# Performance work log

Measured on AMD Instinct MI355X. Metric: run time of the kernel, lower is better.

The kernel has to match this reference:

```python
import jax, jax.numpy as jnp
import numpy as np

B, N, T, D, H, E = 2, 1024, 8, 128, 4, 8192
DH = D // H
NEG_SLOPE = 0.2  # GATv2Conv default negative_slope


def _ln(x, g, b):
    m = jnp.mean(x, -1, keepdims=True)
    v = jnp.mean((x - m) ** 2, -1, keepdims=True)
    return (x - m) * jax.lax.rsqrt(v + 1e-5) * g + b


def _forward(x, edge_index, gat_wl, gat_wr, gat_att, gat_b, in_w, in_b, out_w, out_b,
             ffn_w1, ffn_b1, ffn_w2, ffn_b2, fus_w, fus_b,
             lns_g, lns_b, lnt1_g, lnt1_b, lnt2_g, lnt2_b, lnf_g, lnf_b):
    # ---- spatial branch: GATv2, vectorized over (B, T) instead of python loops ----
    loops = jnp.arange(N)
    src = jnp.concatenate([edge_index[0], loops])  # j: message source (PyG adds self loops)
    dst = jnp.concatenate([edge_index[1], loops])  # i: aggregation target
    xl = jnp.einsum('bntd,de->bnte', x, gat_wl).reshape(B, N, T, H, D)
    xr = jnp.einsum('bntd,de->bnte', x, gat_wr).reshape(B, N, T, H, D)
    ml = xl[:, src]                                  # [B,Et,T,H,D]
    mr = xr[:, dst]
    e = jax.nn.leaky_relu(ml + mr, NEG_SLOPE)
    logits = jnp.einsum('bethd,hd->beth', e, gat_att)
    logits = jnp.moveaxis(logits, 1, 0)              # [Et,B,T,H]
    mx = jax.ops.segment_max(logits, dst, num_segments=N)
    p = jnp.exp(logits - mx[dst])                    # stable edge softmax per dst node
    ssum = jax.ops.segment_sum(p, dst, num_segments=N)
    alpha = p / ssum[dst]                            # [Et,B,T,H]
    msg = alpha[..., None] * jnp.moveaxis(ml, 1, 0)
    agg = jax.ops.segment_sum(msg, dst, num_segments=N)  # [N,B,T,H,D]
    x_sp = jnp.moveaxis(agg.mean(3), 0, 1) + gat_b   # concat=False -> head mean; [B,N,T,D]
    x_sp = _ln(x_sp, lns_g, lns_b)

    # ---- temporal branch: MHA + FFN, vectorized over all B*N nodes ----
    xt = x.reshape(B * N, T, D)
    qkv = xt @ in_w + in_b
    q, k, v = jnp.split(qkv, 3, axis=-1)
    q = q.reshape(B * N, T, H, DH)
    k = k.reshape(B * N, T, H, DH)
    v = v.reshape(B * N, T, H, DH)
    scores = jnp.einsum('bthd,bshd->bhts', q, k) / np.float32(np.sqrt(DH))
    attn = jax.nn.softmax(scores, -1)
    o = jnp.einsum('bhts,bshd->bthd', attn, v).reshape(B * N, T, D)
    o = o @ out_w + out_b
    x1 = _ln(xt + o, lnt1_g, lnt1_b)
    ffn = jax.nn.gelu(x1 @ ffn_w1 + ffn_b1, approximate=False) @ ffn_w2 + ffn_b2
    x_tp = _ln(x1 + ffn, lnt2_g, lnt2_b).reshape(B, N, T, D)

    # ---- gated fusion with residual ----
    g = jax.nn.sigmoid(jnp.concatenate([x_sp, x_tp], -1) @ fus_w + fus_b)
    return _ln(g * x_sp + (1.0 - g) * x_tp + x, lnf_g, lnf_b)


def setup_inputs() -> dict:
    key = jax.random.key(0)
    ks = jax.random.split(key, 12)
    s = 0.05
    f = jnp.float32
    return {
        'x': jax.random.normal(ks[0], (B, N, T, D), f),
        'edge_index': jax.random.randint(ks[1], (2, E), 0, N),
        'gat_wl': jax.random.normal(ks[2], (D, H * D), f) * s,
        'gat_wr': jax.random.normal(ks[3], (D, H * D), f) * s,
        'gat_att': jax.random.normal(ks[4], (H, D), f) * s,
        'gat_b': jnp.zeros((D,), f),
        'in_w': jax.random.normal(ks[5], (D, 3 * D), f) * s,
        'in_b': jnp.zeros((3 * D,), f),
        'out_w': jax.random.normal(ks[6], (D, D), f) * s,
        'out_b': jnp.zeros((D,), f),
        'ffn_w1': jax.random.normal(ks[7], (D, 4 * D), f) * s,
        'ffn_b1': jnp.zeros((4 * D,), f),
        'ffn_w2': jax.random.normal(ks[8], (4 * D, D), f) * s,
        'ffn_b2': jnp.zeros((D,), f),
        'fus_w': jax.random.normal(ks[9], (2 * D, D), f) * s,
        'fus_b': jnp.zeros((D,), f),
        'lns_g': jnp.ones((D,), f), 'lns_b': jnp.zeros((D,), f),
        'lnt1_g': jnp.ones((D,), f), 'lnt1_b': jnp.zeros((D,), f),
        'lnt2_g': jnp.ones((D,), f), 'lnt2_b': jnp.zeros((D,), f),
        'lnf_g': jnp.ones((D,), f), 'lnf_b': jnp.zeros((D,), f),
    }


def reference(x, edge_index, gat_wl, gat_wr, gat_att, gat_b, in_w, in_b, out_w, out_b,
              ffn_w1, ffn_b1, ffn_w2, ffn_b2, fus_w, fus_b,
              lns_g, lns_b, lnt1_g, lnt1_b, lnt2_g, lnt2_b, lnf_g, lnf_b):
    return _forward(x, edge_index, gat_wl, gat_wr, gat_att, gat_b, in_w, in_b, out_w, out_b,
                    ffn_w1, ffn_b1, ffn_w2, ffn_b2, fus_w, fus_b,
                    lns_g, lns_b, lnt1_g, lnt1_b, lnt2_g, lnt2_b, lnf_g, lnf_b)
```

## Files before the change

### kernel.cpp

```cpp
#include <hip/hip_runtime.h>
#include <math.h>

#define B_ 2
#define N_ 1024
#define T_ 8
#define D_ 128
#define H_ 4
#define E_ 8192
#define EN_ 9216
#define M_ 16384

typedef unsigned short u16;
using bf16x8 = __attribute__((ext_vector_type(8))) short;
using f32x4  = __attribute__((ext_vector_type(4))) float;

__device__ __forceinline__ float bf2f(unsigned int u) {
  return __uint_as_float(u << 16);
}
__device__ __forceinline__ u16 f2bf(float f) {
  unsigned int x = __float_as_uint(f);
  x += 0x7fffu + ((x >> 16) & 1u);
  return (u16)(x >> 16);
}
__device__ __forceinline__ void load8f(const u16* p, float* f) {
  uint4 u = *(const uint4*)p;
  f[0]=bf2f(u.x & 0xffffu); f[1]=bf2f(u.x >> 16);
  f[2]=bf2f(u.y & 0xffffu); f[3]=bf2f(u.y >> 16);
  f[4]=bf2f(u.z & 0xffffu); f[5]=bf2f(u.z >> 16);
  f[6]=bf2f(u.w & 0xffffu); f[7]=bf2f(u.w >> 16);
}
__device__ __forceinline__ void unpack8(uint4 u, float* f) {
  f[0]=bf2f(u.x & 0xffffu); f[1]=bf2f(u.x >> 16);
  f[2]=bf2f(u.y & 0xffffu); f[3]=bf2f(u.y >> 16);
  f[4]=bf2f(u.z & 0xffffu); f[5]=bf2f(u.z >> 16);
  f[6]=bf2f(u.w & 0xffffu); f[7]=bf2f(u.w >> 16);
}
__device__ __forceinline__ void gl2lds(const u16* g, u16* l) {
  __builtin_amdgcn_global_load_lds(
      (const __attribute__((address_space(1))) unsigned int*)(const void*)g,
      (__attribute__((address_space(3))) unsigned int*)(void*)l,
      16, 0, 0);
}

__device__ __forceinline__ u16 conv_w_elem(int idx,
    const float* wl, const float* wr, const float* inw, const float* outw,
    const float* f1, const float* f2, const float* fw) {
  const float* src; int base, K, N;
  if      (idx < 65536)  { src = wl;   base = 0;      K = 128; N = 512; }
  else if (idx < 131072) { src = wr;   base = 65536;  K = 128; N = 512; }
  else if (idx < 180224) { src = inw;  base = 131072; K = 128; N = 384; }
  else if (idx < 196608) { src = outw; base = 180224; K = 128; N = 128; }
  else if (idx < 262144) { src = f1;   base = 196608; K = 128; N = 512; }
  else if (idx < 327680) { src = f2;   base = 262144; K = 512; N = 128; }
  else                   { src = fw;   base = 327680; K = 256; N = 128; }
  int o = idx - base;
  int n = o / K, k = o - n * K;
  return f2bf(src[k * N + n]);
}

__global__ __launch_bounds__(1024) void prep_csr_k(const float* __restrict__ x,
    const float* __restrict__ wl, const float* __restrict__ wr,
    const float* __restrict__ inw, const float* __restrict__ outw,
    const float* __restrict__ f1, const float* __restrict__ f2,
    const float* __restrict__ fw,
    u16* __restrict__ XB, u16* __restrict__ WB,
    const int* __restrict__ ei, int* __restrict__ offs, int* __restrict__ srcs) {
  __shared__ int cnt[N_];
  __shared__ int cur[N_];
  int bi = blockIdx.x;
  int tid = threadIdx.x;
  if (bi < 512) {
    int i = (bi * 1024 + tid) * 4;
    float4 v = *(const float4*)&x[i];
    u16 o[4] = {f2bf(v.x), f2bf(v.y), f2bf(v.z), f2bf(v.w)};
    *(ushort4*)&XB[i] = *(ushort4*)o;
    return;
  }
  if (bi < 600) {
    int base = (bi - 512) * 4096 + tid * 4;
#pragma unroll
    for (int j = 0; j < 4; ++j)
      WB[base + j] = conv_w_elem(base + j, wl, wr, inw, outw, f1, f2, fw);
    return;
  }
  cnt[tid] = 0;
  __syncthreads();
  for (int e = tid; e < EN_; e += 1024) {
    int d = (e < E_) ? ei[E_ + e] : (e - E_);
    atomicAdd(&cnt[d], 1);
  }
  __syncthreads();
  int mine = cnt[tid];
  for (int off = 1; off < 1024; off <<= 1) {
    int tv = (tid >= off) ? cnt[tid - off] : 0;
    __syncthreads();
    cnt[tid] += tv;
    __syncthreads();
  }
  int excl = cnt[tid] - mine;
  offs[tid] = excl;
  if (tid == 1023) offs[N_] = cnt[1023];
  cur[tid] = excl;
  __syncthreads();
  for (int e = tid; e < EN_; e += 1024) {
    int d = (e < E_) ? ei[E_ + e] : (e - E_);
    int s = (e < E_) ? ei[e] : (e - E_);
    int pos = atomicAdd(&cur[d], 1);
    srcs[pos] = s;
  }
}

template<int BM, int ACT, int ROUTE>
__device__ __forceinline__ void gemm_tile(int bx, int by,
    const u16* A, int lda, const u16* WT, int K, const float* bias,
    u16* C, int ldc, u16* R0, u16* R1, u16* R2, const float* b2,
    u16* As, u16* Bs) {
  constexpr int MI = BM / 32;
  int tid = threadIdx.x;
  int lane = tid & 63, wid = tid >> 6;
  int lr = lane & 15, lk = lane >> 4;
  int wm = (wid >> 1) * (BM / 2);
  int wn = (wid & 1) * 64;

  u16* Cb; int ldc_; int col0; const float* bias_;
  if (ROUTE) {
    if (bx < 4)      { Cb = R0; ldc_ = 512; col0 = bx * 128;       bias_ = nullptr; }
    else if (bx < 8) { Cb = R1; ldc_ = 512; col0 = (bx - 4) * 128; bias_ = nullptr; }
    else             { Cb = R2; ldc_ = 384; col0 = (bx - 8) * 128; bias_ = b2; }
  } else { Cb = C; ldc_ = ldc; col0 = bx * 128; bias_ = bias; }

  f32x4 acc[MI][4] = {};
  for (int k0 = 0; k0 < K; k0 += 32) {
    __syncthreads();
#pragma unroll
    for (int i = 0; i < BM / 64; ++i) {
      int o = tid * 16 + i * 4096;
      int row = o >> 6;
      int col = (o >> 1) & 31;
      gl2lds(A + (size_t)(by * BM + row) * lda + k0 + col,
             (u16*)((char*)As + wid * 1024 + i * 4096));
    }
#pragma unroll
    for (int i = 0; i < 2; ++i) {
      int o = tid * 16 + i * 4096;
      int nrow = o >> 6;
      int col = (o >> 1) & 31;
      gl2lds(WT + (size_t)(bx * 128 + nrow) * K + k0 + col,
             (u16*)((char*)Bs + wid * 1024 + i * 4096));
    }
    __syncthreads();
    bf16x8 bf[4];
#pragma unroll
    for (int ni = 0; ni < 4; ++ni)
      bf[ni] = *(const bf16x8*)&Bs[(wn + ni * 16 + lr) * 32 + lk * 8];
#pragma unroll
    for (int mi = 0; mi < MI; ++mi) {
      bf16x8 af = *(const bf16x8*)&As[(wm + mi * 16 + lr) * 32 + lk * 8];
#pragma unroll
      for (int ni = 0; ni < 4; ++ni)
        acc[mi][ni] = __builtin_amdgcn_mfma_f32_16x16x32_bf16(af, bf[ni], acc[mi][ni], 0, 0, 0);
    }
  }
  float bc[4];
#pragma unroll
  for (int ni = 0; ni < 4; ++ni)
    bc[ni] = bias_ ? bias_[col0 + wn + ni * 16 + lr] : 0.f;
#pragma unroll
  for (int mi = 0; mi < MI; ++mi) {
#pragma unroll
    for (int r = 0; r < 4; ++r) {
      int row = by * BM + wm + mi * 16 + lk * 4 + r;
#pragma unroll
      for (int ni = 0; ni < 4; ++ni) {
        int col = col0 + wn + ni * 16 + lr;
        float v = acc[mi][ni][r] + bc[ni];
        if (ACT) v = 0.5f * v * (1.f + erff(v * 0.70710678118f));
        Cb[(size_t)row * ldc_ + col] = f2bf(v);
      }
    }
  }
}

template<int EPI>
__device__ __forceinline__ void ln_epilogue(int by, f32x4 (&acc)[2][4],
    const float* bias, const float* xres, const u16* xcat,
    const float* lng, const float* lnb,
    float* o32, u16* o16, int os16, float* rs, float* rq) {
  int tid = threadIdx.x;
  int lane = tid & 63, wid = tid >> 6;
  int lr = lane & 15, lk = lane >> 4;
  int wm = (wid >> 1) * 32, wn = (wid & 1) * 64;
  float bc[4];
#pragma unroll
  for (int ni = 0; ni < 4; ++ni) bc[ni] = bias[wn + ni * 16 + lr];
#pragma unroll
  for (int mi = 0; mi < 2; ++mi) {
#pragma unroll
    for (int r = 0; r < 4; ++r) {
      int row = by * 64 + wm + mi * 16 + lk * 4 + r;
      float s = 0.f, s2 = 0.f;
#pragma unroll
      for (int ni = 0; ni < 4; ++ni) {
        int col = wn + ni * 16 + lr;
        float v = acc[mi][ni][r] + bc[ni];
        if (EPI == 1 || EPI == 2) {
          v += xres[(size_t)row * 128 + col];
        } else {
          float gg = 1.f / (1.f + __expf(-v));
          float xsp = bf2f(xcat[(size_t)row * 256 + col]);
          float xtp = bf2f(xcat[(size_t)row * 256 + 128 + col]);
          v = gg * xsp + (1.f - gg) * xtp + xres[(size_t)row * 128 + col];
        }
        acc[mi][ni][r] = v;
        s += v; s2 += v * v;
      }
      s += __shfl_xor(s, 1, 64); s2 += __shfl_xor(s2, 1, 64);
      s += __shfl_xor(s, 2, 64); s2 += __shfl_xor(s2, 2, 64);
      s += __shfl_xor(s, 4, 64); s2 += __shfl_xor(s2, 4, 64);
      s += __shfl_xor(s, 8, 64); s2 += __shfl_xor(s2, 8, 64);
      if (lr == 0) {
        int rl = wm + mi * 16 + lk * 4 + r;
        rs[rl * 2 + (wid & 1)] = s;
        rq[rl * 2 + (wid & 1)] = s2;
      }
    }
  }
  __syncthreads();
#pragma unroll
  for (int mi = 0; mi < 2; ++mi) {
#pragma unroll
    for (int r = 0; r < 4; ++r) {
      int rl = wm + mi * 16 + lk * 4 + r;
      int row = by * 64 + rl;
      float tot = rs[rl * 2] + rs[rl * 2 + 1];
      float tq = rq[rl * 2] + rq[rl * 2 + 1];
      float mean = tot * (1.f / 128.f);
      float var = tq * (1.f / 128.f) - mean * mean;
      float rinv = rsqrtf(var + 1e-5f);
#pragma unroll
      for (int ni = 0; ni < 4; ++ni) {
        int col = wn + ni * 16 + lr;
        float o = (acc[mi][ni][r] - mean) * rinv * lng[col] + lnb[col];
        if (EPI != 2) o32[(size_t)row * 128 + col] = o;
        if (EPI != 3) o16[(size_t)row * os16 + col] = f2bf(o);
      }
    }
  }
}

__global__ __launch_bounds__(256) void fusion_k(const u16* __restrict__ A,
    const u16* __restrict__ WT, const float* __restrict__ bias,
    const float* __restrict__ xres, const u16* __restrict__ xcat,
    const float* __restrict__ lng, const float* __restrict__ lnb,
    float* __restrict__ o32) {
  __shared__ u16 As[64 * 32];
  __shared__ u16 Bs[128 * 32];
  __shared__ float rs[128], rq[128];
  int by = blockIdx.x;
  int tid = threadIdx.x;
  int lane = tid & 63, wid = tid >> 6;
  int lr = lane & 15, lk = lane >> 4;
  int wm = (wid >> 1) * 32, wn = (wid & 1) * 64;
  const int K = 256;

  f32x4 acc[2][4] = {};
  for (int k0 = 0; k0 < K; k0 += 32) {
    __syncthreads();
    {
      int o = tid * 16;
      gl2lds(A + (size_t)(by * 64 + (o >> 6)) * K + k0 + ((o >> 1) & 31),
             (u16*)((char*)As + wid * 1024));
    }
#pragma unroll
    for (int i = 0; i < 2; ++i) {
      int o = tid * 16 + i * 4096;
      gl2lds(WT + (size_t)(o >> 6) * K + k0 + ((o >> 1) & 31),
             (u16*)((char*)Bs + wid * 1024 + i * 4096));
    }
    __syncthreads();
    bf16x8 bf[4];
#pragma unroll
    for (int ni = 0; ni < 4; ++ni)
      bf[ni] = *(const bf16x8*)&Bs[(wn + ni * 16 + lr) * 32 + lk * 8];
#pragma unroll
    for (int mi = 0; mi < 2; ++mi) {
      bf16x8 af = *(const bf16x8*)&As[(wm + mi * 16 + lr) * 32 + lk * 8];
#pragma unroll
      for (int ni = 0; ni < 4; ++ni)
        acc[mi][ni] = __builtin_amdgcn_mfma_f32_16x16x32_bf16(af, bf[ni], acc[mi][ni], 0, 0, 0);
    }
  }
  ln_epilogue<3>(by, acc, bias, xres, xcat, lng, lnb, o32, nullptr, 0, rs, rq);
}

__global__ __launch_bounds__(256) void proj_k(const u16* __restrict__ XB,
    const u16* __restrict__ WT1, const float* __restrict__ in_b,
    u16* __restrict__ XL, u16* __restrict__ XR, u16* __restrict__ QKV) {
  __shared__ u16 As[128 * 32];
  __shared__ u16 Bs[128 * 32];
  gemm_tile<128, 0, 1>(blockIdx.x, blockIdx.y, XB, 128, WT1, 128, nullptr,
                       nullptr, 0, XL, XR, QKV, in_b, As, Bs);
}

__global__ __launch_bounds__(256) void gat_k(const u16* __restrict__ XL,
    const u16* __restrict__ XR,
    const int* __restrict__ offs, const int* __restrict__ srcs,
    const float* __restrict__ att, const float* __restrict__ gb,
    const float* __restrict__ lng, const float* __restrict__ lnb,
    u16* __restrict__ XCAT) {
  int w = blockIdx.x * 4 + (threadIdx.x >> 6);
  int lane = threadIdx.x & 63;
  int n = w >> 4;
  int b = (w >> 3) & 1;
  int t = w & 7;
  int dd = (lane & 15) * 8;
  size_t tokn = (size_t)(b * N_ + n) * 8 + t;
  size_t rowoff = (size_t)b * (N_ * 8) + t;

  float mr[8], av[8];
  load8f(XR + tokn * 512 + lane * 8, mr);
  *(float4*)&av[0] = *(const float4*)(att + lane * 8);
  *(float4*)&av[4] = *(const float4*)(att + lane * 8 + 4);

  int beg = offs[n], end = offs[n + 1];
  float sH = 0.f;
  float acc[8] = {0.f, 0.f, 0.f, 0.f, 0.f, 0.f, 0.f, 0.f};
  int i = beg;
  uint4 r0 = *(const uint4*)(XL + (rowoff + (size_t)srcs[i] * 8) * 512 + lane * 8);
  uint4 r1 = r0;
  if (i + 1 < end)
    r1 = *(const uint4*)(XL + (rowoff + (size_t)srcs[i + 1] * 8) * 512 + lane * 8);
  while (i + 1 < end) {
    uint4 c0 = r0, c1 = r1;
    if (i + 2 < end)
      r0 = *(const uint4*)(XL + (rowoff + (size_t)srcs[i + 2] * 8) * 512 + lane * 8);
    if (i + 3 < end)
      r1 = *(const uint4*)(XL + (rowoff + (size_t)srcs[i + 3] * 8) * 512 + lane * 8);
    float ml0[8], ml1[8];
    unpack8(c0, ml0);
    unpack8(c1, ml1);
    float d0 = 0.f, d1 = 0.f;
#pragma unroll
    for (int j = 0; j < 8; ++j) {
      float m0 = ml0[j] + mr[j];
      m0 = fmaxf(m0, 0.2f * m0);
      d0 += m0 * av[j];
      float m1 = ml1[j] + mr[j];
      m1 = fmaxf(m1, 0.2f * m1);
      d1 += m1 * av[j];
    }
    d0 += __shfl_xor(d0, 1, 64); d1 += __shfl_xor(d1, 1, 64);
    d0 += __shfl_xor(d0, 2, 64); d1 += __shfl_xor(d1, 2, 64);
    d0 += __shfl_xor(d0, 4, 64); d1 += __shfl_xor(d1, 4, 64);
    d0 += __shfl_xor(d0, 8, 64); d1 += __shfl_xor(d1, 8, 64);
    float p0 = __expf(d0), p1 = __expf(d1);
    sH += p0 + p1;
#pragma unroll
    for (int j = 0; j < 8; ++j) acc[j] += p0 * ml0[j] + p1 * ml1[j];
    i += 2;
  }
  if (i < end) {
    float ml0[8];
    unpack8(r0, ml0);
    float d0 = 0.f;
#pragma unroll
    for (int j = 0; j < 8; ++j) {
      float m0 = ml0[j] + mr[j];
      m0 = fmaxf(m0, 0.2f * m0);
      d0 += m0 * av[j];
    }
    d0 += __shfl_xor(d0, 1, 64);
    d0 += __shfl_xor(d0, 2, 64);
    d0 += __shfl_xor(d0, 4, 64);
    d0 += __shfl_xor(d0, 8, 64);
    float p0 = __expf(d0);
    sH += p0;
#pragma unroll
    for (int j = 0; j < 8; ++j) acc[j] += p0 * ml0[j];
  }
  float invS = 1.f / sH;
#pragma unroll
  for (int j = 0; j < 8; ++j) acc[j] *= invS;
#pragma unroll
  for (int j = 0; j < 8; ++j) {
    acc[j] += __shfl_xor(acc[j], 16, 64);
    acc[j] += __shfl_xor(acc[j], 32, 64);
  }
#pragma unroll
  for (int j = 0; j < 8; ++j) acc[j] = acc[j] * 0.25f + gb[dd + j];
  float s = 0.f, s2 = 0.f;
#pragma unroll
  for (int j = 0; j < 8; ++j) { s += acc[j]; s2 += acc[j] * acc[j]; }
#pragma unroll
  for (int m = 1; m < 16; m <<= 1) {
    s += __shfl_xor(s, m, 64);
    s2 += __shfl_xor(s2, m, 64);
  }
  float mean = s * (1.f / 128.f);
  float var = s2 * (1.f / 128.f) - mean * mean;
  float r = rsqrtf(var + 1e-5f);
  if (lane < 16) {
    u16 ob[8];
#pragma unroll
    for (int j = 0; j < 8; ++j)
      ob[j] = f2bf((acc[j] - mean) * r * lng[dd + j] + lnb[dd + j]);
    *(uint4*)&XCAT[tokn * 256 + dd] = *(uint4*)ob;
  }
}

__global__ __launch_bounds__(256) void attn_oproj_k(const u16* __restrict__ QKV,
    const u16* __restrict__ WTO, const float* __restrict__ out_b,
    const float* __restrict__ x,
    const float* __restrict__ lnt1_g, const float* __restrict__ lnt1_b,
    float* __restrict__ X1, u16* __restrict__ X1B) {
  __shared__ u16 As[4 * 64 * 32];
  __shared__ u16 Bs[4 * 128 * 32];
  __shared__ float rs[128], rq[128];
  int by = blockIdx.x;
  int tid = threadIdx.x;
  int lane = tid & 63, wid = tid >> 6;

#pragma unroll
  for (int i = 0; i < 8; ++i) {
    int o = tid * 16 + i * 4096;
    int c = o >> 13;
    int wb = o & 8191;
    int nrow = wb >> 6;
    int kin = (wb & 63) >> 1;
    gl2lds(WTO + (size_t)nrow * 128 + c * 32 + kin,
           (u16*)((char*)Bs + wid * 1024 + i * 4096));
  }

  int t = lane >> 3, sidx = lane & 7, dg = lane & 7;
  for (int it = 0; it < 8; ++it) {
    int task = wid * 8 + it;
    int bnl = task >> 2, h = task & 3;
    int bn = by * 8 + bnl;
    const u16* base = QKV + (size_t)bn * 8 * 384;
    float va[8][4];
#pragma unroll
    for (int s2 = 0; s2 < 8; ++s2) {
      ushort4 vv = *(const ushort4*)(base + s2 * 384 + 256 + h * 32 + dg * 4);
      va[s2][0] = bf2f(vv.x); va[s2][1] = bf2f(vv.y);
      va[s2][2] = bf2f(vv.z); va[s2][3] = bf2f(vv.w);
    }
    const u16* qp = base + t * 384 + h * 32;
    const u16* kp = base + sidx * 384 + 128 + h * 32;
    float sc = 0.f;
#pragma unroll
    for (int d0 = 0; d0 < 32; d0 += 8) {
      float q[8], k[8];
      load8f(qp + d0, q);
      load8f(kp + d0, k);
#pragma unroll
      for (int j = 0; j < 8; ++j) sc += q[j] * k[j];
    }
    sc *= 0.17677669529663687f;
    float m = sc;
    m = fmaxf(m, __shfl_xor(m, 1, 64));
    m = fmaxf(m, __shfl_xor(m, 2, 64));
    m = fmaxf(m, __shfl_xor(m, 4, 64));
    float p = __expf(sc - m);
    float S = p;
    S += __shfl_xor(S, 1, 64);
    S += __shfl_xor(S, 2, 64);
    S += __shfl_xor(S, 4, 64);
    float alpha = p / S;
    int tb = lane & 56;
    float o0 = 0.f, o1 = 0.f, o2 = 0.f, o3 = 0.f;
#pragma unroll
    for (int s2 = 0; s2 < 8; ++s2) {
      float a = __shfl(alpha, tb + s2, 64);
      o0 += a * va[s2][0];
      o1 += a * va[s2][1];
      o2 += a * va[s2][2];
      o3 += a * va[s2][3];
    }
    u16 ov[4] = {f2bf(o0), f2bf(o1), f2bf(o2), f2bf(o3)};
    int row = bnl * 8 + t;
    *(ushort4*)&As[h * 2048 + row * 32 + dg * 4] = *(ushort4*)ov;
  }
  __syncthreads();

  int lr = lane & 15, lk = lane >> 4;
  int wm = (wid >> 1) * 32, wn = (wid & 1) * 64;
  f32x4 acc[2][4] = {};
#pragma unroll
  for (int c = 0; c < 4; ++c) {
    bf16x8 bf[4];
#pragma unroll
    for (int ni = 0; ni < 4; ++ni)
      bf[ni] = *(const bf16x8*)&Bs[c * 4096 + (wn + ni * 16 + lr) * 32 + lk * 8];
#pragma unroll
    for (int mi = 0; mi < 2; ++mi) {
      bf16x8 af = *(const bf16x8*)&As[c * 2048 + (wm + mi * 16 + lr) * 32 + lk * 8];
#pragma unroll
      for (int ni = 0; ni < 4; ++ni)
        acc[mi][ni] = __builtin_amdgcn_mfma_f32_16x16x32_bf16(af, bf[ni], acc[mi][ni], 0, 0, 0);
    }
  }
  ln_epilogue<1>(by, acc, out_b, x, nullptr, lnt1_g, lnt1_b, X1, X1B, 128, rs, rq);
}

__global__ __launch_bounds__(256) void ffn_fused_k(const u16* __restrict__ X1B,
    const u16* __restrict__ WTF1, const u16* __restrict__ WTF2,
    const float* __restrict__ b1, const float* __restrict__ b2,
    const float* __restrict__ X1,
    const float* __restrict__ lng, const float* __restrict__ lnb,
    u16* __restrict__ XCATr) {
  __shared__ u16 As[64 * 128];
  __shared__ u16 B1s[64 * 128];
  __shared__ u16 B2s[128 * 64];
  __shared__ u16 Hc[2 * 64 * 40];
  __shared__ float rs[128], rq[128];
  int by = blockIdx.x;
  int tid = threadIdx.x;
  int lane = tid & 63, wid = tid >> 6;
  int lr = lane & 15, lk = lane >> 4;

#pragma unroll
  for (int kc = 0; kc < 4; ++kc) {
    gl2lds(X1B + (size_t)(by * 64 + (tid >> 2)) * 128 + kc * 32 + (tid & 3) * 8,
           (u16*)((char*)As + kc * 4096 + wid * 1024));
  }
  int wr0 = (wid >> 1) * 32, wc0 = (wid & 1) * 32;
  int wm = (wid >> 1) * 32, wn = (wid & 1) * 64;
  f32x4 acc2[2][4] = {};
  for (int nc = 0; nc < 8; ++nc) {
    __syncthreads();
#pragma unroll
    for (int kc = 0; kc < 4; ++kc) {
      gl2lds(WTF1 + (size_t)(nc * 64 + (tid >> 2)) * 128 + kc * 32 + (tid & 3) * 8,
             (u16*)((char*)B1s + kc * 4096 + wid * 1024));
    }
#pragma unroll
    for (int i = 0; i < 4; ++i) {
      int o = tid * 16 + i * 4096;
      int kc2l = o >> 13;
      int wb = o & 8191;
      int nrow = wb >> 6;
      int kin = (wb & 63) >> 1;
      gl2lds(WTF2 + (size_t)nrow * 512 + nc * 64 + kc2l * 32 + kin,
             (u16*)((char*)B2s + wid * 1024 + i * 4096));
    }
    __syncthreads();
    f32x4 a1[2][2] = {};
#pragma unroll
    for (int kc = 0; kc < 4; ++kc) {
      bf16x8 bf0 = *(const bf16x8*)&B1s[kc * 2048 + (wc0 + lr) * 32 + lk * 8];
      bf16x8 bf1 = *(const bf16x8*)&B1s[kc * 2048 + (wc0 + 16 + lr) * 32 + lk * 8];
#pragma unroll
      for (int mi = 0; mi < 2; ++mi) {
        bf16x8 af = *(const bf16x8*)&As[kc * 2048 + (wr0 + mi * 16 + lr) * 32 + lk * 8];
        a1[mi][0] = __builtin_amdgcn_mfma_f32_16x16x32_bf16(af, bf0, a1[mi][0], 0, 0, 0);
        a1[mi][1] = __builtin_amdgcn_mfma_f32_16x16x32_bf16(af, bf1, a1[mi][1], 0, 0, 0);
      }
    }
#pragma unroll
    for (int mi = 0; mi < 2; ++mi) {
#pragma unroll
      for (int r = 0; r < 4; ++r) {
        int row = wr0 + mi * 16 + lk * 4 + r;
#pragma unroll
        for (int ni = 0; ni < 2; ++ni) {
          int cl = wc0 + ni * 16 + lr;
          float v = a1[mi][ni][r] + b1[nc * 64 + cl];
          v = 0.5f * v * (1.f + erff(v * 0.70710678118f));
          Hc[(cl >> 5) * 2560 + row * 40 + (cl & 31)] = f2bf(v);
        }
      }
    }
    __syncthreads();
#pragma unroll
    for (int kc2l = 0; kc2l < 2; ++kc2l) {
      bf16x8 bf[4];
#pragma unroll
      for (int ni = 0; ni < 4; ++ni)
        bf[ni] = *(const bf16x8*)&B2s[kc2l * 4096 + (wn + ni * 16 + lr) * 32 + lk * 8];
#pragma unroll
      for (int mi = 0; mi < 2; ++mi) {
        bf16x8 af = *(const bf16x8*)&Hc[kc2l * 2560 + (wm + mi * 16 + lr) * 40 + lk * 8];
#pragma unroll
        for (int ni = 0; ni < 4; ++ni)
          acc2[mi][ni] = __builtin_amdgcn_mfma_f32_16x16x32_bf16(af, bf[ni], acc2[mi][ni], 0, 0, 0);
      }
    }
  }
  __syncthreads();
  ln_epilogue<2>(by, acc2, b2, X1, nullptr, lng, lnb, nullptr, XCATr, 256, rs, rq);
}

extern "C" void kernel_launch(void* const* d_in, const int* in_sizes, int n_in,
                              void* d_out, int out_size, void* d_ws, size_t ws_size,
                              hipStream_t stream) {
  const float* x       = (const float*)d_in[0];
  const int*   ei      = (const int*)d_in[1];
  const float* gat_att = (const float*)d_in[4];
  const float* gat_b   = (const float*)d_in[5];
  const float* in_b    = (const float*)d_in[7];
  const float* out_b   = (const float*)d_in[9];
  const float* ffn_b1  = (const float*)d_in[11];
  const float* ffn_b2  = (const float*)d_in[13];
  const float* fus_b   = (const float*)d_in[15];
  const float* lns_g   = (const float*)d_in[16];
  const float* lns_b   = (const float*)d_in[17];
  const float* lnt1_g  = (const float*)d_in[18];
  const float* lnt1_b  = (const float*)d_in[19];
  const float* lnt2_g  = (const float*)d_in[20];
  const float* lnt2_b  = (const float*)d_in[21];
  const float* lnf_g   = (const float*)d_in[22];
  const float* lnf_b   = (const float*)d_in[23];

  char* ws = (char*)d_ws;
  u16*   WB    = (u16*)ws;
  u16*   WTO   = WB + 180224;
  u16*   WTF1  = WB + 196608;
  u16*   WTF2  = WB + 262144;
  u16*   WTFUS = WB + 327680;
  int*   OFFS  = (int*)(ws + 3145728);
  int*   SRCS  = (int*)(ws + 3153920);
  u16*   XB   = (u16*)(ws + 4194304);
  u16*   XL   = (u16*)(ws + 8388608);
  u16*   XR   = (u16*)(ws + 25165824);
  float* X1   = (float*)(ws + 41943040);
  u16*   QKV  = (u16*)(ws + 50331648);
  u16*   X1B  = (u16*)(ws + 62914560);
  u16*   XCAT = (u16*)(ws + 67108864);

  prep_csr_k<<<dim3(601), dim3(1024), 0, stream>>>(x,
      (const float*)d_in[2], (const float*)d_in[3], (const float*)d_in[6],
      (const float*)d_in[8], (const float*)d_in[10], (const float*)d_in[12],
      (const float*)d_in[14], XB, WB, ei, OFFS, SRCS);

  proj_k<<<dim3(11, 128), dim3(256), 0, stream>>>(XB, WB, in_b, XL, XR, QKV);

  gat_k<<<dim3(4096), dim3(256), 0, stream>>>(XL, XR, OFFS, SRCS,
      gat_att, gat_b, lns_g, lns_b, XCAT);

  attn_oproj_k<<<dim3(256), dim3(256), 0, stream>>>(QKV, WTO, out_b, x,
      lnt1_g, lnt1_b, X1, X1B);

  ffn_fused_k<<<dim3(256), dim3(256), 0, stream>>>(X1B, WTF1, WTF2,
      ffn_b1, ffn_b2, X1, lnt2_g, lnt2_b, XCAT + 128);

  fusion_k<<<dim3(256), dim3(256), 0, stream>>>(XCAT, WTFUS, fus_b, x, XCAT,
      lnf_g, lnf_b, (float*)d_out);
}
```

Baseline: 221.2 us.

## Store GAT projections in (b,t)-major layout and map blocks to XCDs per slice

The projection GEMM now writes XL and XR rows remapped so each (batch, time) slice is a contiguous [N,512] block. The GAT kernel reassigns block indices so each XCD works on a fixed (b,t) slice, which keeps the gathered neighbor rows in a compact region that stays resident in that XCD's L2. This is meant to cut scattered global reads during the edge gather. It relies on blocks being dispatched round-robin across the XCDs, and any other readers of XL/XR must agree on the new layout.

```diff
diff --git a/kernel.cpp b/kernel.cpp
--- a/kernel.cpp
+++ b/kernel.cpp
@@ -40,6 +40,10 @@
       (const __attribute__((address_space(1))) unsigned int*)(const void*)g,
       (__attribute__((address_space(3))) unsigned int*)(void*)l,
       16, 0, 0);
+}
+
+__device__ __forceinline__ size_t bt_row(int r) {
+  return (size_t)(((r >> 13) << 3) | (r & 7)) * 1024 + ((r >> 3) & 1023);
 }
 
 __device__ __forceinline__ u16 conv_w_elem(int idx,
@@ -122,12 +126,12 @@
   int wm = (wid >> 1) * (BM / 2);
   int wn = (wid & 1) * 64;
 
-  u16* Cb; int ldc_; int col0; const float* bias_;
+  u16* Cb; int ldc_; int col0; const float* bias_; int remap;
   if (ROUTE) {
-    if (bx < 4)      { Cb = R0; ldc_ = 512; col0 = bx * 128;       bias_ = nullptr; }
-    else if (bx < 8) { Cb = R1; ldc_ = 512; col0 = (bx - 4) * 128; bias_ = nullptr; }
-    else             { Cb = R2; ldc_ = 384; col0 = (bx - 8) * 128; bias_ = b2; }
-  } else { Cb = C; ldc_ = ldc; col0 = bx * 128; bias_ = bias; }
+    if (bx < 4)      { Cb = R0; ldc_ = 512; col0 = bx * 128;       bias_ = nullptr; remap = 1; }
+    else if (bx < 8) { Cb = R1; ldc_ = 512; col0 = (bx - 4) * 128; bias_ = nullptr; remap = 1; }
+    else             { Cb = R2; ldc_ = 384; col0 = (bx - 8) * 128; bias_ = b2;      remap = 0; }
+  } else { Cb = C; ldc_ = ldc; col0 = bx * 128; bias_ = bias; remap = 0; }
 
   f32x4 acc[MI][4] = {};
   for (int k0 = 0; k0 < K; k0 += 32) {
@@ -170,12 +174,13 @@
 #pragma unroll
     for (int r = 0; r < 4; ++r) {
       int row = by * BM + wm + mi * 16 + lk * 4 + r;
+      size_t orow = (ROUTE && remap) ? bt_row(row) : (size_t)row;
 #pragma unroll
       for (int ni = 0; ni < 4; ++ni) {
         int col = col0 + wn + ni * 16 + lr;
         float v = acc[mi][ni][r] + bc[ni];
         if (ACT) v = 0.5f * v * (1.f + erff(v * 0.70710678118f));
-        Cb[(size_t)row * ldc_ + col] = f2bf(v);
+        Cb[orow * ldc_ + col] = f2bf(v);
       }
     }
   }
@@ -308,17 +313,20 @@
     const float* __restrict__ att, const float* __restrict__ gb,
     const float* __restrict__ lng, const float* __restrict__ lnb,
     u16* __restrict__ XCAT) {
-  int w = blockIdx.x * 4 + (threadIdx.x >> 6);
+  int bid = blockIdx.x;
   int lane = threadIdx.x & 63;
-  int n = w >> 4;
-  int b = (w >> 3) & 1;
-  int t = w & 7;
+  int wid = threadIdx.x >> 6;
+  int xcd = bid & 7;
+  int slot = bid >> 3;
+  int p = ((slot >> 8) << 3) | xcd;
+  int n = (slot & 255) * 4 + wid;
+  int b = p >> 3, t = p & 7;
   int dd = (lane & 15) * 8;
   size_t tokn = (size_t)(b * N_ + n) * 8 + t;
-  size_t rowoff = (size_t)b * (N_ * 8) + t;
+  const u16* XLs = XL + (size_t)p * 1024 * 512;
 
   float mr[8], av[8];
-  load8f(XR + tokn * 512 + lane * 8, mr);
+  load8f(XR + ((size_t)p * 1024 + n) * 512 + lane * 8, mr);
   *(float4*)&av[0] = *(const float4*)(att + lane * 8);
   *(float4*)&av[4] = *(const float4*)(att + lane * 8 + 4);
 
@@ -326,16 +334,16 @@
   float sH = 0.f;
   float acc[8] = {0.f, 0.f, 0.f, 0.f, 0.f, 0.f, 0.f, 0.f};
   int i = beg;
-  uint4 r0 = *(const uint4*)(XL + (rowoff + (size_t)srcs[i] * 8) * 512 + lane * 8);
+  uint4 r0 = *(const uint4*)(XLs + (size_t)srcs[i] * 512 + lane * 8);
   uint4 r1 = r0;
   if (i + 1 < end)
-    r1 = *(const uint4*)(XL + (rowoff + (size_t)srcs[i + 1] * 8) * 512 + lane * 8);
+    r1 = *(const uint4*)(XLs + (size_t)srcs[i + 1] * 512 + lane * 8);
   while (i + 1 < end) {
     uint4 c0 = r0, c1 = r1;
     if (i + 2 < end)
-      r0 = *(const uint4*)(XL + (rowoff + (size_t)srcs[i + 2] * 8) * 512 + lane * 8);
+      r0 = *(const uint4*)(XLs + (size_t)srcs[i + 2] * 512 + lane * 8);
     if (i + 3 < end)
-      r1 = *(const uint4*)(XL + (rowoff + (size_t)srcs[i + 3] * 8) * 512 + lane * 8);
+      r1 = *(const uint4*)(XLs + (size_t)srcs[i + 3] * 512 + lane * 8);
     float ml0[8], ml1[8];
     unpack8(c0, ml0);
     unpack8(c1, ml1);
```

Result: no change. 220.1 us (-0.5%).
